# Optimization experiments

Measured on AMD Instinct MI355X. Metric: run time of the kernel, lower is better.

Reference implementation:

```python
import jax, jax.numpy as jnp
import numpy as np

B, N, D = 8, 4096, 1024
NC, NU = 8, 32            # core / universal experts (num_experts=16, occ_factor=1/4)
E = NC + NU               # 40 total experts
S = 2                     # slots per expert
HC, HU = 4 * D, D         # core hidden = 4*dim, occ hidden = 4*occ_factor*dim = dim
L2_EPS = 1e-6
LN_EPS = 1e-5


def l2norm(x):
    n = jnp.sqrt(jnp.sum(x * x, axis=-1, keepdims=True))
    return x * (1.0 / (n + L2_EPS))


def layernorm(x, g, b):
    mu = jnp.mean(x, axis=-1, keepdims=True)
    var = jnp.mean((x - mu) ** 2, axis=-1, keepdims=True)
    return (x - mu) / jnp.sqrt(var + LN_EPS) * g + b


def entmax15(z):
    # exact 1.5-entmax over last axis (sorted algorithm, Peters et al. 2019)
    z = z / 2.0
    z = z - jnp.max(z, axis=-1, keepdims=True)
    zs = -jnp.sort(-z, axis=-1)                      # descending
    K = z.shape[-1]
    k = jnp.arange(1, K + 1, dtype=z.dtype)
    mean = jnp.cumsum(zs, axis=-1) / k
    meansq = jnp.cumsum(zs * zs, axis=-1) / k
    ss = k * (meansq - mean * mean)
    delta = jnp.maximum((1.0 - ss) / k, 1e-12)
    tau = mean - jnp.sqrt(delta)
    support = jnp.sum((tau <= zs).astype(jnp.int32), axis=-1, keepdims=True)
    tau_star = jnp.take_along_axis(tau, support - 1, axis=-1)
    return jnp.maximum(z - tau_star, 0.0) ** 2


def setup_inputs() -> dict:
    key = jax.random.key(0)
    ks = jax.random.split(key, 8)
    return {
        "x": jax.random.normal(ks[0], (B, N, D), jnp.float32),
        "attn_weight": jax.random.uniform(ks[1], (B, 128), jnp.float32),
        "phi": jax.random.normal(ks[2], (E, S, D), jnp.float32) * 0.02,
        "key_gamma": jnp.ones((D,), jnp.float32),
        "key_beta": jnp.zeros((D,), jnp.float32),
        "query_gamma": jnp.ones((D,), jnp.float32),
        "query_beta": jnp.zeros((D,), jnp.float32),
        "ln_gamma": jnp.ones((D,), jnp.float32),
        "ln_beta": jnp.zeros((D,), jnp.float32),
        "scale0": jnp.asarray(0.5, jnp.float32),
        "scale1": jnp.asarray(0.5, jnp.float32),
        "core_w1": jax.random.normal(ks[3], (NC, D, HC), jnp.float32) * (D ** -0.5),
        "core_b1": jnp.zeros((NC, HC), jnp.float32),
        "core_w2": jax.random.normal(ks[4], (NC, HC, D), jnp.float32) * (HC ** -0.5),
        "core_b2": jnp.zeros((NC, D), jnp.float32),
        "occ_w1": jax.random.normal(ks[5], (NU, D, HU), jnp.float32) * (D ** -0.5),
        "occ_b1": jnp.zeros((NU, HU), jnp.float32),
        "occ_w2": jax.random.normal(ks[6], (NU, HU, D), jnp.float32) * (HU ** -0.5),
        "occ_b2": jnp.zeros((NU, D), jnp.float32),
    }


def _expert_mlp(s, w1, b1, w2, b2):
    # s: [b, e, s, d]; per-expert 2-layer MLP with exact GELU
    h = jax.nn.gelu(jnp.einsum('besd,edh->besh', s, w1) + b1[None, :, None, :], approximate=False)
    return jnp.einsum('besh,ehd->besd', h, w2) + b2[None, :, None, :]


def reference(x, attn_weight, phi, key_gamma, key_beta, query_gamma, query_beta,
              ln_gamma, ln_beta, scale0, scale1,
              core_w1, core_b1, core_w2, core_b2,
              occ_w1, occ_b1, occ_w2, occ_b2):
    # keys: OffsetScale then l2norm
    k = l2norm(x * key_gamma + key_beta)
    # queries: OffsetScale -> LayerNorm -> l2norm on phi
    q = layernorm(phi * query_gamma + query_beta, ln_gamma, ln_beta)
    q = l2norm(q)
    logits = jnp.einsum('bnd,esd->bnes', k, q)                      # [B,N,E,S]
    core_mask = (jnp.arange(E) < NC)[None, None, :, None]
    adjusted = jnp.where(core_mask, logits, jnp.asarray(-10000.0, logits.dtype))
    dispatch = jax.nn.softmax(adjusted / scale0, axis=2)            # softmax over experts
    combine = entmax15((adjusted / scale1).reshape(B, N, E * S))    # [B,N,E*S]
    slots = jnp.einsum('bnd,bnes->besd', x, dispatch)               # [B,E,S,D]
    core_out = _expert_mlp(slots[:, :NC], core_w1, core_b1, core_w2, core_b2)
    occ_out = _expert_mlp(slots[:, NC:], occ_w1, occ_b1, occ_w2, occ_b2)
    out = jnp.concatenate([core_out, occ_out], axis=1).reshape(B, E * S, D)
    return jnp.einsum('bsd,bns->bnd', out, combine)                 # [B,N,D]
```

## Files before the change

### kernel.cpp

```cpp
#include <hip/hip_runtime.h>
#include <hip/hip_bf16.h>

#define B_ 8
#define N_ 4096
#define D_ 1024

#define AS1 __attribute__((address_space(1)))
#define AS3 __attribute__((address_space(3)))
__device__ __forceinline__ void gld16(const float* g, float* l) {
    __builtin_amdgcn_global_load_lds((const AS1 void*)g, (AS3 void*)l, 16, 0, 0);
}

__global__ __launch_bounds__(64) void k_prep(
    const float* __restrict__ phi, const float* __restrict__ qg, const float* __restrict__ qb,
    const float* __restrict__ lng, const float* __restrict__ lnb,
    const float* __restrict__ kg, const float* __restrict__ kb,
    float* __restrict__ qk, float* __restrict__ cj, float* __restrict__ wbuf)
{
    int r = blockIdx.x;
    int lane = threadIdx.x;
    if (r == 16) {
        float cacc = 0.f;
#pragma unroll
        for (int c = 0; c < 16; ++c) {
            int i = c * 64 + lane;
            float g = kg[i], b = kb[i];
            wbuf[i] = g * g;
            wbuf[1024 + i] = 2.0f * g * b;
            cacc += b * b;
        }
#pragma unroll
        for (int m = 32; m; m >>= 1) cacc += __shfl_xor(cacc, m);
        if (lane == 0) wbuf[2048] = cacc;
        return;
    }
    const float* pr = phi + (size_t)r * D_;
    float v[16];
    float s1 = 0.f;
#pragma unroll
    for (int c = 0; c < 16; ++c) {
        int i = c * 64 + lane;
        v[c] = pr[i] * qg[i] + qb[i];
        s1 += v[c];
    }
#pragma unroll
    for (int m = 32; m; m >>= 1) s1 += __shfl_xor(s1, m);
    float mu = s1 * (1.0f / D_);
    float s2 = 0.f;
#pragma unroll
    for (int c = 0; c < 16; ++c) { float dd = v[c] - mu; s2 += dd * dd; }
#pragma unroll
    for (int m = 32; m; m >>= 1) s2 += __shfl_xor(s2, m);
    float var = s2 * (1.0f / D_);
    float inv = 1.0f / sqrtf(var + 1e-5f);
    float u[16];
    float s3 = 0.f;
#pragma unroll
    for (int c = 0; c < 16; ++c) {
        int i = c * 64 + lane;
        u[c] = (v[c] - mu) * inv * lng[i] + lnb[i];
        s3 += u[c] * u[c];
    }
#pragma unroll
    for (int m = 32; m; m >>= 1) s3 += __shfl_xor(s3, m);
    float rn = 1.0f / (sqrtf(s3) + 1e-6f);
    float cacc = 0.f;
#pragma unroll
    for (int c = 0; c < 16; ++c) {
        int i = c * 64 + lane;
        float qv = u[c] * rn;
        qk[(size_t)r * D_ + i] = qv * kg[i];
        cacc += qv * kb[i];
    }
#pragma unroll
    for (int m = 32; m; m >>= 1) cacc += __shfl_xor(cacc, m);
    if (lane == 0) cj[r] = cacc;
}

__global__ __launch_bounds__(256) void k_fused(
    const float* __restrict__ x, const float* __restrict__ qk,
    const float* __restrict__ wbuf, const float* __restrict__ cj,
    const float* __restrict__ s0p,
    float* __restrict__ lgbuf, float* __restrict__ spart)
{
    __shared__ float smem[6336];
    float* xs   = smem;
    float* qs   = smem + 4096;
    float* wsd  = smem + 5120;
    float* sums = smem + 5248;
    float* disp = smem + 4096;

    int tid = threadIdx.x;
    int tok0 = blockIdx.x * 64;
    int tok32 = tid & 31, gg = tid >> 5;
    int wid = tid >> 6;

    float acc[2][17];
#pragma unroll
    for (int u = 0; u < 2; ++u)
#pragma unroll
        for (int v = 0; v < 17; ++v) acc[u][v] = 0.f;

    int st[4], sg[4];
#pragma unroll
    for (int i = 0; i < 4; ++i) {
        int s = i * 256 + tid;
        int tok = s >> 4, sc = s & 15;
        st[i] = tok;
        sg[i] = (sc ^ (tok & 15)) << 2;
    }

#pragma unroll 1
    for (int dc = 0; dc < 16; ++dc) {
#pragma unroll
        for (int i = 0; i < 4; ++i)
            gld16(x + (size_t)(tok0 + st[i]) * D_ + dc * 64 + sg[i],
                  &xs[(i * 256 + wid * 64) * 4]);
        gld16(qk + (size_t)(tid >> 4) * D_ + dc * 64 + ((tid & 15) << 2),
              &qs[wid * 256]);
        if (tid < 128) wsd[tid] = wbuf[(size_t)(tid >> 6) * 1024 + dc * 64 + (tid & 63)];
        __syncthreads();

        const float* qp = qs + gg * 8;
        const float* wp = wsd + gg * 8;
#pragma unroll
        for (int dl4 = 0; dl4 < 2; ++dl4) {
            int c = gg * 2 + dl4;
            int t0 = tok32, t1 = 32 + tok32;
            float4 xv0 = *(const float4*)(&xs[(t0 * 16 + (c ^ (t0 & 15))) * 4]);
            float4 xv1 = *(const float4*)(&xs[(t1 * 16 + (c ^ (t1 & 15))) * 4]);
            float4 w2v = *(const float4*)(wp + dl4 * 4);
            float4 w1v = *(const float4*)(wp + 64 + dl4 * 4);
            acc[0][16] += (w2v.x * xv0.x + w1v.x) * xv0.x + (w2v.y * xv0.y + w1v.y) * xv0.y
                        + (w2v.z * xv0.z + w1v.z) * xv0.z + (w2v.w * xv0.w + w1v.w) * xv0.w;
            acc[1][16] += (w2v.x * xv1.x + w1v.x) * xv1.x + (w2v.y * xv1.y + w1v.y) * xv1.y
                        + (w2v.z * xv1.z + w1v.z) * xv1.z + (w2v.w * xv1.w + w1v.w) * xv1.w;
#pragma unroll
            for (int j = 0; j < 16; ++j) {
                float4 q4 = *(const float4*)(qp + j * 64 + dl4 * 4);
                acc[0][j] += xv0.x * q4.x + xv0.y * q4.y + xv0.z * q4.z + xv0.w * q4.w;
                acc[1][j] += xv1.x * q4.x + xv1.y * q4.y + xv1.z * q4.z + xv1.w * q4.w;
            }
        }
        __syncthreads();
    }

    float* red = smem;
#pragma unroll
    for (int half = 0; half < 2; ++half) {
        __syncthreads();
#pragma unroll
        for (int v = 0; v < 17; ++v) red[(tok32 * 17 + v) * 8 + gg] = acc[half][v];
        __syncthreads();
#pragma unroll
        for (int it = 0; it < 3; ++it) {
            int idx = tid + it * 256;
            if (idx < 544) {
                float4 p0 = *(const float4*)(red + idx * 8);
                float4 p1v = *(const float4*)(red + idx * 8 + 4);
                float sum = ((p0.x + p0.y) + (p0.z + p0.w)) + ((p1v.x + p1v.y) + (p1v.z + p1v.w));
                int t = idx / 17, v = idx - t * 17;
                lgbuf[(size_t)(tok0 + half * 32 + t) * 20 + v] = sum;
                sums[(half * 32 + t) * 17 + v] = sum;
            }
        }
    }
    __syncthreads();

    if (tid < 64) {
        const float* sp = sums + tid * 17;
        float ss = sp[16] + wbuf[2048];
        float rn = 1.0f / (sqrtf(ss) + 1e-6f);
        float inv0 = 1.0f / s0p[0];
        float lg[16];
#pragma unroll
        for (int j = 0; j < 16; ++j) lg[j] = (sp[j] + cj[j]) * rn;
        float dsp[16];
#pragma unroll
        for (int sl = 0; sl < 2; ++sl) {
            float a[8], m = -1e30f;
#pragma unroll
            for (int ee = 0; ee < 8; ++ee) { a[ee] = lg[2 * ee + sl] * inv0; m = fmaxf(m, a[ee]); }
            float den = 0.f;
#pragma unroll
            for (int ee = 0; ee < 8; ++ee) { a[ee] = expf(a[ee] - m); den += a[ee]; }
            float r = 1.0f / den;
#pragma unroll
            for (int ee = 0; ee < 8; ++ee) dsp[2 * ee + sl] = a[ee] * r;
        }
#pragma unroll
        for (int q4i = 0; q4i < 4; ++q4i)
            *(float4*)(&disp[tid * 16 + q4i * 4]) =
                make_float4(dsp[q4i * 4 + 0], dsp[q4i * 4 + 1], dsp[q4i * 4 + 2], dsp[q4i * 4 + 3]);
    }
    __syncthreads();

    const float* xp = x + (size_t)tok0 * D_ + tid * 4;
    float4 acc2[16];
#pragma unroll
    for (int j = 0; j < 16; ++j) { acc2[j].x = 0.f; acc2[j].y = 0.f; acc2[j].z = 0.f; acc2[j].w = 0.f; }
#pragma unroll 8
    for (int n = 0; n < 64; ++n) {
        float4 xv = *(const float4*)(xp + (size_t)n * D_);
        const float4* q4 = (const float4*)(disp + n * 16);
        float4 s0 = q4[0], s1 = q4[1], s2 = q4[2], s3 = q4[3];
        acc2[0].x  += s0.x * xv.x; acc2[0].y  += s0.x * xv.y; acc2[0].z  += s0.x * xv.z; acc2[0].w  += s0.x * xv.w;
        acc2[1].x  += s0.y * xv.x; acc2[1].y  += s0.y * xv.y; acc2[1].z  += s0.y * xv.z; acc2[1].w  += s0.y * xv.w;
        acc2[2].x  += s0.z * xv.x; acc2[2].y  += s0.z * xv.y; acc2[2].z  += s0.z * xv.z; acc2[2].w  += s0.z * xv.w;
        acc2[3].x  += s0.w * xv.x; acc2[3].y  += s0.w * xv.y; acc2[3].z  += s0.w * xv.z; acc2[3].w  += s0.w * xv.w;
        acc2[4].x  += s1.x * xv.x; acc2[4].y  += s1.x * xv.y; acc2[4].z  += s1.x * xv.z; acc2[4].w  += s1.x * xv.w;
        acc2[5].x  += s1.y * xv.x; acc2[5].y  += s1.y * xv.y; acc2[5].z  += s1.y * xv.z; acc2[5].w  += s1.y * xv.w;
        acc2[6].x  += s1.z * xv.x; acc2[6].y  += s1.z * xv.y; acc2[6].z  += s1.z * xv.z; acc2[6].w  += s1.z * xv.w;
        acc2[7].x  += s1.w * xv.x; acc2[7].y  += s1.w * xv.y; acc2[7].z  += s1.w * xv.z; acc2[7].w  += s1.w * xv.w;
        acc2[8].x  += s2.x * xv.x; acc2[8].y  += s2.x * xv.y; acc2[8].z  += s2.x * xv.z; acc2[8].w  += s2.x * xv.w;
        acc2[9].x  += s2.y * xv.x; acc2[9].y  += s2.y * xv.y; acc2[9].z  += s2.y * xv.z; acc2[9].w  += s2.y * xv.w;
        acc2[10].x += s2.z * xv.x; acc2[10].y += s2.z * xv.y; acc2[10].z += s2.z * xv.z; acc2[10].w += s2.z * xv.w;
        acc2[11].x += s2.w * xv.x; acc2[11].y += s2.w * xv.y; acc2[11].z += s2.w * xv.z; acc2[11].w += s2.w * xv.w;
        acc2[12].x += s3.x * xv.x; acc2[12].y += s3.x * xv.y; acc2[12].z += s3.x * xv.z; acc2[12].w += s3.x * xv.w;
        acc2[13].x += s3.y * xv.x; acc2[13].y += s3.y * xv.y; acc2[13].z += s3.y * xv.z; acc2[13].w += s3.y * xv.w;
        acc2[14].x += s3.z * xv.x; acc2[14].y += s3.z * xv.y; acc2[14].z += s3.z * xv.z; acc2[14].w += s3.z * xv.w;
        acc2[15].x += s3.w * xv.x; acc2[15].y += s3.w * xv.y; acc2[15].z += s3.w * xv.z; acc2[15].w += s3.w * xv.w;
    }
    float* op = spart + ((size_t)blockIdx.x * 16) * 1024 + tid * 4;
#pragma unroll
    for (int j = 0; j < 16; ++j)
        *(float4*)(op + (size_t)j * 1024) = acc2[j];
}

__global__ __launch_bounds__(64) void k_epi(
    const float* __restrict__ lgbuf, const float* __restrict__ cj,
    const float* __restrict__ wbuf, const float* __restrict__ s1p,
    float* __restrict__ combine)
{
    int tok = blockIdx.x * 64 + threadIdx.x;
    const float* lp = lgbuf + (size_t)tok * 20;
    float s[17];
    float4 q0 = *(const float4*)(lp + 0);
    float4 q1 = *(const float4*)(lp + 4);
    float4 q2 = *(const float4*)(lp + 8);
    float4 q3 = *(const float4*)(lp + 12);
    s[0] = q0.x; s[1] = q0.y; s[2] = q0.z; s[3] = q0.w;
    s[4] = q1.x; s[5] = q1.y; s[6] = q1.z; s[7] = q1.w;
    s[8] = q2.x; s[9] = q2.y; s[10] = q2.z; s[11] = q2.w;
    s[12] = q3.x; s[13] = q3.y; s[14] = q3.z; s[15] = q3.w;
    s[16] = lp[16];

    float ss = s[16] + wbuf[2048];
    float rn = 1.0f / (sqrtf(ss) + 1e-6f);
    float inv1h = 0.5f / s1p[0];
    float lg[16];
#pragma unroll
    for (int j = 0; j < 16; ++j) lg[j] = (s[j] + cj[j]) * rn;

    float z[16], zmax = -1e30f;
#pragma unroll
    for (int j = 0; j < 16; ++j) { z[j] = lg[j] * inv1h; zmax = fmaxf(zmax, z[j]); }
#pragma unroll
    for (int j = 0; j < 16; ++j) z[j] -= zmax;
    float zsr[16];
#pragma unroll
    for (int j = 0; j < 16; ++j) zsr[j] = z[j];
#pragma unroll
    for (int rr = 0; rr < 16; ++rr) {
#pragma unroll
        for (int jj = (rr & 1); jj + 1 < 16; jj += 2) {
            float aa = zsr[jj], bb = zsr[jj + 1];
            zsr[jj] = fmaxf(aa, bb);
            zsr[jj + 1] = fminf(aa, bb);
        }
    }
    float cs = 0.f, css = 0.f, tau_star = 0.f;
#pragma unroll
    for (int kk = 1; kk <= 16; ++kk) {
        cs += zsr[kk - 1];
        css += zsr[kk - 1] * zsr[kk - 1];
        float fk = (float)kk;
        float mean = cs / fk, msq = css / fk;
        float ssv = fk * (msq - mean * mean);
        float delta = fmaxf((1.0f - ssv) / fk, 1e-12f);
        float tau = mean - sqrtf(delta);
        tau_star = (tau <= zsr[kk - 1]) ? tau : tau_star;
    }
    float4* cw = (float4*)(combine + (size_t)tok * 16);
#pragma unroll
    for (int q4i = 0; q4i < 4; ++q4i) {
        float4 cv;
        float t0 = fmaxf(z[q4i * 4 + 0] - tau_star, 0.f);
        float t1 = fmaxf(z[q4i * 4 + 1] - tau_star, 0.f);
        float t2 = fmaxf(z[q4i * 4 + 2] - tau_star, 0.f);
        float t3 = fmaxf(z[q4i * 4 + 3] - tau_star, 0.f);
        cv.x = t0 * t0; cv.y = t1 * t1; cv.z = t2 * t2; cv.w = t3 * t3;
        cw[q4i] = cv;
    }
}

__global__ __launch_bounds__(256) void k_slots_reduce(
    const float* __restrict__ spart, float* __restrict__ slotsT)
{
    int j = blockIdx.x, b = blockIdx.y;
    int tid = threadIdx.x;
    const float* p = spart + ((size_t)(b * 64) * 16 + j) * 1024 + tid * 4;
    float4 s; s.x = 0.f; s.y = 0.f; s.z = 0.f; s.w = 0.f;
#pragma unroll 8
    for (int nc = 0; nc < 64; ++nc) {
        float4 v = *(const float4*)(p + (size_t)nc * 16384);
        s.x += v.x; s.y += v.y; s.z += v.z; s.w += v.w;
    }
    int e = j >> 1, sl = j & 1;
    int t = b * 2 + sl;
    float* o = slotsT + ((size_t)e * 1024 + tid * 4) * 16 + t;
    o[0] = s.x; o[16] = s.y; o[32] = s.z; o[48] = s.w;
}

__global__ __launch_bounds__(256) void k_mlp1(
    const float* __restrict__ w1, const float* __restrict__ slotsT,
    float* __restrict__ p1)
{
    __shared__ float sm[1024];
    int cc = blockIdx.x, ks = blockIdx.y, e = blockIdx.z;
    int tid = threadIdx.x;
    int k0 = ks * 64;
    int col = cc * 1024 + tid * 4;
    ((float4*)sm)[tid] = ((const float4*)(slotsT + ((size_t)e * 1024 + k0) * 16))[tid];
    __syncthreads();

    const float* wp = w1 + (size_t)e * 1024 * 4096 + (size_t)k0 * 4096 + col;
    float4 acc[16];
#pragma unroll
    for (int t = 0; t < 16; ++t) { acc[t].x = 0.f; acc[t].y = 0.f; acc[t].z = 0.f; acc[t].w = 0.f; }
#pragma unroll 8
    for (int kk = 0; kk < 64; ++kk) {
        float4 w = *(const float4*)(wp + (size_t)kk * 4096);
        const float4* q4 = (const float4*)(sm + kk * 16);
        float4 s0 = q4[0], s1 = q4[1], s2 = q4[2], s3 = q4[3];
        acc[0].x  += s0.x * w.x; acc[0].y  += s0.x * w.y; acc[0].z  += s0.x * w.z; acc[0].w  += s0.x * w.w;
        acc[1].x  += s0.y * w.x; acc[1].y  += s0.y * w.y; acc[1].z  += s0.y * w.z; acc[1].w  += s0.y * w.w;
        acc[2].x  += s0.z * w.x; acc[2].y  += s0.z * w.y; acc[2].z  += s0.z * w.z; acc[2].w  += s0.z * w.w;
        acc[3].x  += s0.w * w.x; acc[3].y  += s0.w * w.y; acc[3].z  += s0.w * w.z; acc[3].w  += s0.w * w.w;
        acc[4].x  += s1.x * w.x; acc[4].y  += s1.x * w.y; acc[4].z  += s1.x * w.z; acc[4].w  += s1.x * w.w;
        acc[5].x  += s1.y * w.x; acc[5].y  += s1.y * w.y; acc[5].z  += s1.y * w.z; acc[5].w  += s1.y * w.w;
        acc[6].x  += s1.z * w.x; acc[6].y  += s1.z * w.y; acc[6].z  += s1.z * w.z; acc[6].w  += s1.z * w.w;
        acc[7].x  += s1.w * w.x; acc[7].y  += s1.w * w.y; acc[7].z  += s1.w * w.z; acc[7].w  += s1.w * w.w;
        acc[8].x  += s2.x * w.x; acc[8].y  += s2.x * w.y; acc[8].z  += s2.x * w.z; acc[8].w  += s2.x * w.w;
        acc[9].x  += s2.y * w.x; acc[9].y  += s2.y * w.y; acc[9].z  += s2.y * w.z; acc[9].w  += s2.y * w.w;
        acc[10].x += s2.z * w.x; acc[10].y += s2.z * w.y; acc[10].z += s2.z * w.z; acc[10].w += s2.z * w.w;
        acc[11].x += s2.w * w.x; acc[11].y += s2.w * w.y; acc[11].z += s2.w * w.z; acc[11].w += s2.w * w.w;
        acc[12].x += s3.x * w.x; acc[12].y += s3.x * w.y; acc[12].z += s3.x * w.z; acc[12].w += s3.x * w.w;
        acc[13].x += s3.y * w.x; acc[13].y += s3.y * w.y; acc[13].z += s3.y * w.z; acc[13].w += s3.y * w.w;
        acc[14].x += s3.z * w.x; acc[14].y += s3.z * w.y; acc[14].z += s3.z * w.z; acc[14].w += s3.z * w.w;
        acc[15].x += s3.w * w.x; acc[15].y += s3.w * w.y; acc[15].z += s3.w * w.z; acc[15].w += s3.w * w.w;
    }
    float av0[16], av1[16], av2[16], av3[16];
#pragma unroll
    for (int t = 0; t < 16; ++t) { av0[t] = acc[t].x; av1[t] = acc[t].y; av2[t] = acc[t].z; av3[t] = acc[t].w; }
    float* op = p1 + (((size_t)ks * 8 + e) * 4096 + col) * 16;
#pragma unroll
    for (int q = 0; q < 4; ++q) {
        *(float4*)(op + 0 * 16 + q * 4) = make_float4(av0[q*4+0], av0[q*4+1], av0[q*4+2], av0[q*4+3]);
        *(float4*)(op + 1 * 16 + q * 4) = make_float4(av1[q*4+0], av1[q*4+1], av1[q*4+2], av1[q*4+3]);
        *(float4*)(op + 2 * 16 + q * 4) = make_float4(av2[q*4+0], av2[q*4+1], av2[q*4+2], av2[q*4+3]);
        *(float4*)(op + 3 * 16 + q * 4) = make_float4(av3[q*4+0], av3[q*4+1], av3[q*4+2], av3[q*4+3]);
    }
}

__global__ __launch_bounds__(256) void k_mlp2f(
    const float* __restrict__ w2, const float* __restrict__ p1,
    const float* __restrict__ b1, float* __restrict__ p2)
{
    __shared__ float sm[1024];
    int ks = blockIdx.x, e = blockIdx.y;
    int tid = threadIdx.x;
    int k0 = ks * 64;
    int col = tid * 4;

    {
        int fidx = tid;
        const float* pp = p1 + (size_t)e * 65536 + (size_t)k0 * 16 + fidx * 4;
        float4 s; s.x = 0.f; s.y = 0.f; s.z = 0.f; s.w = 0.f;
#pragma unroll
        for (int ksp = 0; ksp < 16; ++ksp) {
            float4 v = *(const float4*)(pp + (size_t)ksp * 524288);
            s.x += v.x; s.y += v.y; s.z += v.z; s.w += v.w;
        }
        int colh = k0 + (fidx >> 2);
        float bb = b1[(size_t)e * 4096 + colh];
        s.x += bb; s.y += bb; s.z += bb; s.w += bb;
        s.x = 0.5f * s.x * (1.0f + erff(s.x * 0.70710678118654752f));
        s.y = 0.5f * s.y * (1.0f + erff(s.y * 0.70710678118654752f));
        s.z = 0.5f * s.z * (1.0f + erff(s.z * 0.70710678118654752f));
        s.w = 0.5f * s.w * (1.0f + erff(s.w * 0.70710678118654752f));
        *(float4*)(&sm[fidx * 4]) = s;
    }
    __syncthreads();

    const float* wp = w2 + (size_t)e * 4096 * 1024 + (size_t)k0 * 1024 + col;
    float4 acc[16];
#pragma unroll
    for (int t = 0; t < 16; ++t) { acc[t].x = 0.f; acc[t].y = 0.f; acc[t].z = 0.f; acc[t].w = 0.f; }
#pragma unroll 8
    for (int kk = 0; kk < 64; ++kk) {
        float4 w = *(const float4*)(wp + (size_t)kk * 1024);
        const float4* q4 = (const float4*)(sm + kk * 16);
        float4 s0 = q4[0], s1 = q4[1], s2 = q4[2], s3 = q4[3];
        acc[0].x  += s0.x * w.x; acc[0].y  += s0.x * w.y; acc[0].z  += s0.x * w.z; acc[0].w  += s0.x * w.w;
        acc[1].x  += s0.y * w.x; acc[1].y  += s0.y * w.y; acc[1].z  += s0.y * w.z; acc[1].w  += s0.y * w.w;
        acc[2].x  += s0.z * w.x; acc[2].y  += s0.z * w.y; acc[2].z  += s0.z * w.z; acc[2].w  += s0.z * w.w;
        acc[3].x  += s0.w * w.x; acc[3].y  += s0.w * w.y; acc[3].z  += s0.w * w.z; acc[3].w  += s0.w * w.w;
        acc[4].x  += s1.x * w.x; acc[4].y  += s1.x * w.y; acc[4].z  += s1.x * w.z; acc[4].w  += s1.x * w.w;
        acc[5].x  += s1.y * w.x; acc[5].y  += s1.y * w.y; acc[5].z  += s1.y * w.z; acc[5].w  += s1.y * w.w;
        acc[6].x  += s1.z * w.x; acc[6].y  += s1.z * w.y; acc[6].z  += s1.z * w.z; acc[6].w  += s1.z * w.w;
        acc[7].x  += s1.w * w.x; acc[7].y  += s1.w * w.y; acc[7].z  += s1.w * w.z; acc[7].w  += s1.w * w.w;
        acc[8].x  += s2.x * w.x; acc[8].y  += s2.x * w.y; acc[8].z  += s2.x * w.z; acc[8].w  += s2.x * w.w;
        acc[9].x  += s2.y * w.x; acc[9].y  += s2.y * w.y; acc[9].z  += s2.y * w.z; acc[9].w  += s2.y * w.w;
        acc[10].x += s2.z * w.x; acc[10].y += s2.z * w.y; acc[10].z += s2.z * w.z; acc[10].w += s2.z * w.w;
        acc[11].x += s2.w * w.x; acc[11].y += s2.w * w.y; acc[11].z += s2.w * w.z; acc[11].w += s2.w * w.w;
        acc[12].x += s3.x * w.x; acc[12].y += s3.x * w.y; acc[12].z += s3.x * w.z; acc[12].w += s3.x * w.w;
        acc[13].x += s3.y * w.x; acc[13].y += s3.y * w.y; acc[13].z += s3.y * w.z; acc[13].w += s3.y * w.w;
        acc[14].x += s3.z * w.x; acc[14].y += s3.z * w.y; acc[14].z += s3.z * w.z; acc[14].w += s3.z * w.w;
        acc[15].x += s3.w * w.x; acc[15].y += s3.w * w.y; acc[15].z += s3.w * w.z; acc[15].w += s3.w * w.w;
    }
    float av0[16], av1[16], av2[16], av3[16];
#pragma unroll
    for (int t = 0; t < 16; ++t) { av0[t] = acc[t].x; av1[t] = acc[t].y; av2[t] = acc[t].z; av3[t] = acc[t].w; }
    float* op = p2 + (((size_t)ks * 8 + e) * 1024 + col) * 16;
#pragma unroll
    for (int q = 0; q < 4; ++q) {
        *(float4*)(op + 0 * 16 + q * 4) = make_float4(av0[q*4+0], av0[q*4+1], av0[q*4+2], av0[q*4+3]);
        *(float4*)(op + 1 * 16 + q * 4) = make_float4(av1[q*4+0], av1[q*4+1], av1[q*4+2], av1[q*4+3]);
        *(float4*)(op + 2 * 16 + q * 4) = make_float4(av2[q*4+0], av2[q*4+1], av2[q*4+2], av2[q*4+3]);
        *(float4*)(op + 3 * 16 + q * 4) = make_float4(av3[q*4+0], av3[q*4+1], av3[q*4+2], av3[q*4+3]);
    }
}

__global__ __launch_bounds__(256) void k_red2(
    const float* __restrict__ p2, const float* __restrict__ b2,
    float* __restrict__ co)
{
    int idx = blockIdx.x * 256 + threadIdx.x;
    int q = idx & 3, d = (idx >> 2) & 1023, e = idx >> 12;
    const float* p = p2 + ((size_t)e * 1024 + d) * 16 + q * 4;
    float4 s; s.x = 0.f; s.y = 0.f; s.z = 0.f; s.w = 0.f;
#pragma unroll 8
    for (int ks = 0; ks < 64; ++ks) {
        float4 v = *(const float4*)(p + (size_t)ks * 131072);
        s.x += v.x; s.y += v.y; s.z += v.z; s.w += v.w;
    }
    float bb = b2[(size_t)e * 1024 + d];
    float vv[4] = { s.x + bb, s.y + bb, s.z + bb, s.w + bb };
#pragma unroll
    for (int u = 0; u < 4; ++u) {
        int t = q * 4 + u;
        int b = t >> 1, sl = t & 1;
        co[((size_t)b * 16 + e * 2 + sl) * 1024 + d] = vv[u];
    }
}

__global__ __launch_bounds__(256) void k_out(
    const float* __restrict__ co, const float* __restrict__ combine,
    float* __restrict__ out)
{
    __shared__ float sm[1024];
    int b = blockIdx.y, tile = blockIdx.x;
    int tid = threadIdx.x;
    ((float4*)sm)[tid] = ((const float4*)(combine + ((size_t)b * N_ + tile * 64) * 16))[tid];
    float4 cv[16];
#pragma unroll
    for (int j = 0; j < 16; ++j)
        cv[j] = ((const float4*)(co + ((size_t)b * 16 + j) * 1024))[tid];
    __syncthreads();
    float4* ob = (float4*)(out + ((size_t)b * N_ + tile * 64) * 1024) + tid;
#pragma unroll 2
    for (int it = 0; it < 64; ++it) {
        const float* cm = sm + it * 16;
        float4 acc; acc.x = 0.f; acc.y = 0.f; acc.z = 0.f; acc.w = 0.f;
#pragma unroll
        for (int j = 0; j < 16; ++j) {
            float wj = cm[j];
            acc.x += wj * cv[j].x; acc.y += wj * cv[j].y;
            acc.z += wj * cv[j].z; acc.w += wj * cv[j].w;
        }
        ob[(size_t)it * 256] = acc;
    }
}

extern "C" void kernel_launch(void* const* d_in, const int* in_sizes, int n_in,
                              void* d_out, int out_size, void* d_ws, size_t ws_size,
                              hipStream_t stream)
{
    const float* x   = (const float*)d_in[0];
    const float* phi = (const float*)d_in[2];
    const float* kg  = (const float*)d_in[3];
    const float* kb  = (const float*)d_in[4];
    const float* qg  = (const float*)d_in[5];
    const float* qb  = (const float*)d_in[6];
    const float* lng = (const float*)d_in[7];
    const float* lnb = (const float*)d_in[8];
    const float* s0  = (const float*)d_in[9];
    const float* s1  = (const float*)d_in[10];
    const float* w1  = (const float*)d_in[11];
    const float* b1  = (const float*)d_in[12];
    const float* w2  = (const float*)d_in[13];
    const float* b2  = (const float*)d_in[14];

    float* out = (float*)d_out;
    float* ws  = (float*)d_ws;

    float* qk       = ws;
    float* cj       = qk + 16384;
    float* wbuf     = cj + 16;
    float* combine  = wbuf + 2064;
    float* slotsT   = combine + 524288;
    float* co       = slotsT + 131072;
    float* lgbuf    = co + 131072;
    float* arenaA   = lgbuf + 655360;
    float* arenaB   = arenaA + 8388608;
    float* spart    = arenaA;
    float* p1       = arenaA;
    float* p2       = arenaB;

    k_prep        <<<dim3(17),        dim3(64),  0, stream>>>(phi, qg, qb, lng, lnb, kg, kb, qk, cj, wbuf);
    k_fused       <<<dim3(512),       dim3(256), 0, stream>>>(x, qk, wbuf, cj, s0, lgbuf, spart);
    k_epi         <<<dim3(512),       dim3(64),  0, stream>>>(lgbuf, cj, wbuf, s1, combine);
    k_slots_reduce<<<dim3(16, 8),     dim3(256), 0, stream>>>(spart, slotsT);
    k_mlp1        <<<dim3(4, 16, 8),  dim3(256), 0, stream>>>(w1, slotsT, p1);
    k_mlp2f       <<<dim3(64, 8),     dim3(256), 0, stream>>>(w2, p1, b1, p2);
    k_red2        <<<dim3(128),       dim3(256), 0, stream>>>(p2, b2, co);
    k_out         <<<dim3(64, 8),     dim3(256), 0, stream>>>(co, combine, out);
}
```

Measured before the change: 217.6 us.

## Preload all queries to LDS once and stream x directly from global in logits kernel

The logits kernel now loads the full 16x1024 query matrix and the weight vectors into LDS once per block, instead of reloading a slice every d-chunk. x is read straight from global memory into registers, with each thread owning 4 tokens across a 4-wide d-slice. This removes the per-chunk barriers and the x staging through LDS. The cost is a cross-thread reduction over 16 partials instead of 8, more registers, and about 72KB of LDS per block, which may cut occupancy.

```diff
diff --git a/kernel.cpp b/kernel.cpp
--- a/kernel.cpp
+++ b/kernel.cpp
@@ -83,89 +83,85 @@
     const float* __restrict__ s0p,
     float* __restrict__ lgbuf, float* __restrict__ spart)
 {
-    __shared__ float smem[6336];
-    float* xs   = smem;
-    float* qs   = smem + 4096;
-    float* wsd  = smem + 5120;
-    float* sums = smem + 5248;
-    float* disp = smem + 4096;
+    __shared__ float smem[18436];
+    float* qs   = smem;
+    float* wsd  = smem + 16384;
+    float* red  = smem;
+    float* sums = smem + 8704;
+    float* disp = smem + 9792;
 
     int tid = threadIdx.x;
     int tok0 = blockIdx.x * 64;
-    int tok32 = tid & 31, gg = tid >> 5;
     int wid = tid >> 6;
-
-    float acc[2][17];
-#pragma unroll
-    for (int u = 0; u < 2; ++u)
-#pragma unroll
-        for (int v = 0; v < 17; ++v) acc[u][v] = 0.f;
-
-    int st[4], sg[4];
-#pragma unroll
-    for (int i = 0; i < 4; ++i) {
-        int s = i * 256 + tid;
-        int tok = s >> 4, sc = s & 15;
-        st[i] = tok;
-        sg[i] = (sc ^ (tok & 15)) << 2;
-    }
-
-#pragma unroll 1
+    int r0 = tid >> 4;
+    int c4 = (tid & 15) * 4;
+
+#pragma unroll
+    for (int i = 0; i < 16; ++i)
+        gld16(qk + (size_t)(i * 256 + tid) * 4, &qs[(i * 256 + wid * 64) * 4]);
+#pragma unroll
+    for (int i = 0; i < 2; ++i)
+        gld16(wbuf + (size_t)(i * 256 + tid) * 4, &wsd[(i * 256 + wid * 64) * 4]);
+    __syncthreads();
+
+    float acc[4][17];
+#pragma unroll
+    for (int i = 0; i < 4; ++i)
+#pragma unroll
+        for (int v = 0; v < 17; ++v) acc[i][v] = 0.f;
+
+#pragma unroll 2
     for (int dc = 0; dc < 16; ++dc) {
+        float4 xv[4];
 #pragma unroll
         for (int i = 0; i < 4; ++i)
-            gld16(x + (size_t)(tok0 + st[i]) * D_ + dc * 64 + sg[i],
-                  &xs[(i * 256 + wid * 64) * 4]);
-        gld16(qk + (size_t)(tid >> 4) * D_ + dc * 64 + ((tid & 15) << 2),
-              &qs[wid * 256]);
-        if (tid < 128) wsd[tid] = wbuf[(size_t)(tid >> 6) * 1024 + dc * 64 + (tid & 63)];
-        __syncthreads();
-
-        const float* qp = qs + gg * 8;
-        const float* wp = wsd + gg * 8;
-#pragma unroll
-        for (int dl4 = 0; dl4 < 2; ++dl4) {
-            int c = gg * 2 + dl4;
-            int t0 = tok32, t1 = 32 + tok32;
-            float4 xv0 = *(const float4*)(&xs[(t0 * 16 + (c ^ (t0 & 15))) * 4]);
-            float4 xv1 = *(const float4*)(&xs[(t1 * 16 + (c ^ (t1 & 15))) * 4]);
-            float4 w2v = *(const float4*)(wp + dl4 * 4);
-            float4 w1v = *(const float4*)(wp + 64 + dl4 * 4);
-            acc[0][16] += (w2v.x * xv0.x + w1v.x) * xv0.x + (w2v.y * xv0.y + w1v.y) * xv0.y
-                        + (w2v.z * xv0.z + w1v.z) * xv0.z + (w2v.w * xv0.w + w1v.w) * xv0.w;
-            acc[1][16] += (w2v.x * xv1.x + w1v.x) * xv1.x + (w2v.y * xv1.y + w1v.y) * xv1.y
-                        + (w2v.z * xv1.z + w1v.z) * xv1.z + (w2v.w * xv1.w + w1v.w) * xv1.w;
-#pragma unroll
-            for (int j = 0; j < 16; ++j) {
-                float4 q4 = *(const float4*)(qp + j * 64 + dl4 * 4);
-                acc[0][j] += xv0.x * q4.x + xv0.y * q4.y + xv0.z * q4.z + xv0.w * q4.w;
-                acc[1][j] += xv1.x * q4.x + xv1.y * q4.y + xv1.z * q4.z + xv1.w * q4.w;
-            }
-        }
-        __syncthreads();
-    }
-
-    float* red = smem;
+            xv[i] = *(const float4*)(x + (size_t)(tok0 + i * 16 + r0) * D_ + dc * 64 + c4);
+        float4 w2v = *(const float4*)(wsd + dc * 64 + c4);
+        float4 w1v = *(const float4*)(wsd + 1024 + dc * 64 + c4);
+#pragma unroll
+        for (int i = 0; i < 4; ++i)
+            acc[i][16] += (w2v.x * xv[i].x + w1v.x) * xv[i].x
+                        + (w2v.y * xv[i].y + w1v.y) * xv[i].y
+                        + (w2v.z * xv[i].z + w1v.z) * xv[i].z
+                        + (w2v.w * xv[i].w + w1v.w) * xv[i].w;
+        const float* qb = qs + dc * 64 + c4;
+#pragma unroll
+        for (int j = 0; j < 16; ++j) {
+            float4 q4 = *(const float4*)(qb + j * 1024);
+#pragma unroll
+            for (int i = 0; i < 4; ++i)
+                acc[i][j] += xv[i].x * q4.x + xv[i].y * q4.y
+                           + xv[i].z * q4.z + xv[i].w * q4.w;
+        }
+    }
+    __syncthreads();
+
 #pragma unroll
     for (int half = 0; half < 2; ++half) {
-        __syncthreads();
-#pragma unroll
-        for (int v = 0; v < 17; ++v) red[(tok32 * 17 + v) * 8 + gg] = acc[half][v];
+#pragma unroll
+        for (int u = 0; u < 2; ++u) {
+            int i = half * 2 + u;
+            int rr = u * 16 + r0;
+#pragma unroll
+            for (int v = 0; v < 17; ++v)
+                red[(rr * 17 + v) * 16 + (tid & 15)] = acc[i][v];
+        }
         __syncthreads();
 #pragma unroll
         for (int it = 0; it < 3; ++it) {
             int idx = tid + it * 256;
             if (idx < 544) {
-                float4 p0 = *(const float4*)(red + idx * 8);
-                float4 p1v = *(const float4*)(red + idx * 8 + 4);
-                float sum = ((p0.x + p0.y) + (p0.z + p0.w)) + ((p1v.x + p1v.y) + (p1v.z + p1v.w));
+                const float4* p = (const float4*)(red + idx * 16);
+                float4 a = p[0], b = p[1], cq = p[2], dq = p[3];
+                float sum = (((a.x + a.y) + (a.z + a.w)) + ((b.x + b.y) + (b.z + b.w)))
+                          + (((cq.x + cq.y) + (cq.z + cq.w)) + ((dq.x + dq.y) + (dq.z + dq.w)));
                 int t = idx / 17, v = idx - t * 17;
                 lgbuf[(size_t)(tok0 + half * 32 + t) * 20 + v] = sum;
                 sums[(half * 32 + t) * 17 + v] = sum;
             }
         }
-    }
-    __syncthreads();
+        __syncthreads();
+    }
 
     if (tid < 64) {
         const float* sp = sums + tid * 17;
```

After: 255.7 us. +17.5%, slower.
